# Kernel optimization log

Hardware: AMD Instinct MI355X
Metric: run time of the kernel (lower is better)

The kernel has to match this reference:

```python
import jax, jax.numpy as jnp
import numpy as np

D_MODEL = 1024
N_HEADS = 16
D_K = D_MODEL // N_HEADS
LN_EPS = 1e-5


def setup_inputs() -> dict:
    key = jax.random.key(0)
    ks = jax.random.split(key, 8)
    B, Sq, Skv = 2, 2048, 2048
    scale = 1.0 / np.sqrt(D_MODEL)
    return {
        "query": jax.random.normal(ks[0], (B, Sq, D_MODEL), dtype=jnp.float32),
        "key_value": jax.random.normal(ks[1], (B, Skv, D_MODEL), dtype=jnp.float32),
        "W_qkv": jax.random.normal(ks[2], (3 * D_MODEL, D_MODEL), dtype=jnp.float32) * scale,
        "b_qkv": jax.random.normal(ks[3], (3 * D_MODEL,), dtype=jnp.float32) * 0.01,
        "W_o": jax.random.normal(ks[4], (D_MODEL, D_MODEL), dtype=jnp.float32) * scale,
        "b_o": jax.random.normal(ks[5], (D_MODEL,), dtype=jnp.float32) * 0.01,
        "ln_gamma": jnp.ones((D_MODEL,), dtype=jnp.float32),
        "ln_beta": jnp.zeros((D_MODEL,), dtype=jnp.float32),
    }


def _attention(query, key_value, W_qkv, b_qkv, W_o, b_o, ln_gamma, ln_beta):
    B, Sq, _ = query.shape
    Skv = key_value.shape[1]
    # Q from query rows of qkv_proj; K,V from key_value rows (slice weights -> same
    # math as projecting then slicing, without the discarded 2/3 and 1/3 compute).
    Wq, Wk, Wv = W_qkv[:D_MODEL], W_qkv[D_MODEL:2 * D_MODEL], W_qkv[2 * D_MODEL:]
    bq, bk, bv = b_qkv[:D_MODEL], b_qkv[D_MODEL:2 * D_MODEL], b_qkv[2 * D_MODEL:]
    Q = (query @ Wq.T + bq).reshape(B, Sq, N_HEADS, D_K).transpose(0, 2, 1, 3)
    K = (key_value @ Wk.T + bk).reshape(B, Skv, N_HEADS, D_K).transpose(0, 2, 1, 3)
    V = (key_value @ Wv.T + bv).reshape(B, Skv, N_HEADS, D_K).transpose(0, 2, 1, 3)
    # fp32 attention (original forces float32 inside autocast(enabled=False))
    scores = jnp.einsum('bhqd,bhkd->bhqk', Q.astype(jnp.float32), K.astype(jnp.float32))
    scores = scores / np.sqrt(D_K)
    attn = jax.nn.softmax(scores, axis=-1)  # dropout is identity at inference
    context = jnp.einsum('bhqk,bhkd->bhqd', attn, V.astype(jnp.float32)).astype(query.dtype)
    context = context.transpose(0, 2, 1, 3).reshape(B, Sq, D_MODEL)
    output = context @ W_o.T + b_o
    # residual + LayerNorm
    x = output + query
    mu = jnp.mean(x, axis=-1, keepdims=True)
    var = jnp.mean(jnp.square(x - mu), axis=-1, keepdims=True)
    return (x - mu) / jnp.sqrt(var + LN_EPS) * ln_gamma + ln_beta


def reference(query, key_value, W_qkv, b_qkv, W_o, b_o, ln_gamma, ln_beta):
    return _attention(query, key_value, W_qkv, b_qkv, W_o, b_o, ln_gamma, ln_beta)
```

## Files before the change

### kernel.cpp

```cpp
#include <hip/hip_runtime.h>
#include <hip/hip_bf16.h>

typedef __attribute__((ext_vector_type(4))) float f32x4;
typedef __attribute__((ext_vector_type(16))) float f32x16;
typedef __attribute__((ext_vector_type(8))) __bf16 bf16x8;
typedef __attribute__((ext_vector_type(2))) __bf16 bf16x2;

#define DEV __device__ __forceinline__

DEV unsigned short f2bf(float f) {
    union { float f; unsigned u; } x; x.f = f;
    unsigned r = x.u + 0x7fffu + ((x.u >> 16) & 1u);
    return (unsigned short)(r >> 16);
}

DEV unsigned packbf(float a, float b) {
    union { bf16x2 h; unsigned u; } t;
    t.h[0] = (__bf16)a; t.h[1] = (__bf16)b;
    return t.u;
}

DEV float bflo(unsigned u) { union { unsigned u; float f; } x; x.u = u << 16; return x.f; }
DEV float bfhi(unsigned u) { union { unsigned u; float f; } x; x.u = u & 0xffff0000u; return x.f; }

DEV void gload16(const void* g, void* l) {
    __builtin_amdgcn_global_load_lds(
        (const __attribute__((address_space(1))) void*)g,
        (__attribute__((address_space(3))) void*)l, 16, 0, 0);
}

#define PLSWAP(a, b) asm("v_permlane32_swap_b32 %0, %1" : "+v"(a), "+v"(b))

DEV bf16x8 ldsfrag(const unsigned short* base, int row, int kcol) {
    int byte = (row << 7) + (kcol << 1);
    byte ^= (row & 7) << 4;
    return *reinterpret_cast<const bf16x8*>(reinterpret_cast<const char*>(base) + byte);
}

__global__ __launch_bounds__(256) void cvt_all(
    const float* __restrict__ q, const float* __restrict__ kv,
    const float* __restrict__ wq, const float* __restrict__ wo,
    unsigned short* __restrict__ qb, unsigned short* __restrict__ kvb,
    unsigned short* __restrict__ wqb, unsigned short* __restrict__ wob)
{
    int i = blockIdx.x * 256 + threadIdx.x;
    const float* s; unsigned short* d; int o;
    if (i < 2097152) {
        if (i < 1048576) { s = q;  d = qb;  o = i; }
        else             { s = kv; d = kvb; o = i - 1048576; }
    } else {
        if (i < 2883584) { s = wq; d = wqb; o = i - 2097152; }
        else             { s = wo; d = wob; o = i - 2883584; }
    }
    f32x4 v = *reinterpret_cast<const f32x4*>(s + (size_t)o * 4);
    ushort4 u;
    u.x = f2bf(v.x); u.y = f2bf(v.y); u.z = f2bf(v.z); u.w = f2bf(v.w);
    *reinterpret_cast<ushort4*>(d + (size_t)o * 4) = u;
}

__global__ __launch_bounds__(256) void gemm_qkv(
    const unsigned short* __restrict__ Aq,
    const unsigned short* __restrict__ Akv,
    const unsigned short* __restrict__ W,
    const float* __restrict__ bias,
    unsigned short* __restrict__ QP,
    unsigned short* __restrict__ KP,
    unsigned short* __restrict__ VP)
{
    __shared__ unsigned short lA[2][128 * 64];
    __shared__ unsigned short lB[2][128 * 64];
    int xcd = blockIdx.x & 7, idx = blockIdx.x >> 3;
    int bm = ((xcd >> 1) << 3) + (idx & 7);
    int bn = (xcd & 1) * 12 + (idx >> 3);
    int m0 = bm * 128, n0 = bn * 128;
    const unsigned short* A = (bn < 8) ? Aq : Akv;
    int tid = threadIdx.x, lane = tid & 63, wv = tid >> 6;
    int wm = (wv >> 1) * 64, wn = (wv & 1) * 64;
    int cg = lane >> 4, cl = lane & 15;

    const unsigned short* sA[4];
    const unsigned short* sB[4];
#pragma unroll
    for (int p = 0; p < 4; ++p) {
        int o = p * 4096 + tid * 16;
        int r = o >> 7;
        int c = ((o ^ ((r & 7) << 4)) >> 1) & 63;
        sA[p] = A + (size_t)(m0 + r) * 1024 + c;
        sB[p] = W + (size_t)(n0 + r) * 1024 + c;
    }
    const int dl = wv * 1024;

    auto STAGE = [&](int buf, int k0) {
#pragma unroll
        for (int p = 0; p < 4; ++p) {
            gload16(sA[p] + k0, (char*)lA[buf] + p * 4096 + dl);
            gload16(sB[p] + k0, (char*)lB[buf] + p * 4096 + dl);
        }
    };

    f32x4 acc[4][4] = {};

    STAGE(0, 0);
    for (int kt = 0; kt < 16; ++kt) {
        const int cur = kt & 1;
        if (kt < 15) {
            STAGE(cur ^ 1, (kt + 1) * 64);
            asm volatile("s_waitcnt vmcnt(8)" ::: "memory");
        } else {
            asm volatile("s_waitcnt vmcnt(0)" ::: "memory");
        }
        __builtin_amdgcn_s_barrier();
#pragma unroll
        for (int ks = 0; ks < 2; ++ks) {
            bf16x8 af[4], bfr[4];
#pragma unroll
            for (int i = 0; i < 4; ++i) af[i] = ldsfrag(lA[cur], wm + i * 16 + cl, ks * 32 + cg * 8);
#pragma unroll
            for (int j = 0; j < 4; ++j) bfr[j] = ldsfrag(lB[cur], wn + j * 16 + cl, ks * 32 + cg * 8);
#pragma unroll
            for (int i = 0; i < 4; ++i)
#pragma unroll
                for (int j = 0; j < 4; ++j)
                    acc[i][j] = __builtin_amdgcn_mfma_f32_16x16x32_bf16(af[i], bfr[j], acc[i][j], 0, 0, 0);
        }
        asm volatile("s_waitcnt lgkmcnt(0)" ::: "memory");
        __builtin_amdgcn_s_barrier();
    }

    unsigned short* img = (unsigned short*)lA;
    const int which = (bn >= 16) ? 2 : (bn >= 8 ? 1 : 0);
    const float scale = (which == 0) ? 0.18033688f : 1.0f;

#pragma unroll
    for (int j = 0; j < 4; ++j) {
        int nn = wn + j * 16 + cl;
        int d = nn & 63, chunk = nn >> 6;
        float bv = bias[n0 + nn];
#pragma unroll
        for (int i = 0; i < 4; ++i) {
#pragma unroll
            for (int r = 0; r < 4; ++r) {
                int mm = wm + i * 16 + cg * 4 + r;
                float v = (acc[i][j][r] + bv) * scale;
                int off;
                if (which < 2)
                    off = ((mm >> 5) * 4 + (d >> 4)) * 512
                        + (((d >> 3) & 1) * 32 + (mm & 31)) * 8 + (d & 7);
                else
                    off = (((mm >> 6) * 2 + (d >> 5)) * 4 + ((mm >> 4) & 3)) * 512
                        + (((mm >> 3) & 1) * 32 + (d & 31)) * 8 + (mm & 7);
                img[chunk * 8192 + off] = f2bf(v);
            }
        }
    }
    __syncthreads();

    int bb = m0 >> 11, s0 = m0 & 2047;
    int h0 = (bn & 7) * 2;
    unsigned short* dst[2];
#pragma unroll
    for (int c = 0; c < 2; ++c) {
        int bh = bb * 16 + h0 + c;
        if (which == 0)      dst[c] = QP + ((size_t)bh * 64 + (s0 >> 5)) * 2048;
        else if (which == 1) dst[c] = KP + ((size_t)bh * 64 + (s0 >> 5)) * 2048;
        else                 dst[c] = VP + ((size_t)bh * 32 + (s0 >> 6)) * 4096;
    }
#pragma unroll
    for (int c = 0; c < 2; ++c)
#pragma unroll
        for (int k = 0; k < 4; ++k) {
            int e = (k * 256 + tid) * 8;
            *reinterpret_cast<uint4*>(dst[c] + e) =
                *reinterpret_cast<const uint4*>(img + c * 8192 + e);
        }
}

__global__ __launch_bounds__(256, 2) void attn(
    const unsigned short* __restrict__ QP,
    const unsigned short* __restrict__ KP,
    const unsigned short* __restrict__ VP,
    unsigned short* __restrict__ OP,
    float2* __restrict__ ML)
{
    int swz = (blockIdx.x & 7) * 64 + (blockIdx.x >> 3);
    int bh = swz >> 4;
    int qc = (swz >> 1) & 7;
    int spl = swz & 1;
    int tid = threadIdx.x, lane = tid & 63, wv = tid >> 6;
    int ql = lane & 31, hh = lane >> 5;
    int qs = qc * 256 + wv * 64;
    const unsigned short* kp = KP + (size_t)bh * 131072 + lane * 8;
    const unsigned short* vp = VP + (size_t)bh * 131072 + lane * 8;
    const int tbase = spl * 16;

    bf16x8 qfA[4], qfB[4];
    {
        const unsigned short* qpA = QP + ((size_t)(bh * 64 + (qs >> 5)) * 4) * 512 + lane * 8;
#pragma unroll
        for (int ks = 0; ks < 4; ++ks) {
            qfA[ks] = *reinterpret_cast<const bf16x8*>(qpA + ks * 512);
            qfB[ks] = *reinterpret_cast<const bf16x8*>(qpA + 2048 + ks * 512);
        }
    }

    bf16x8 ka[4], kc[4], va[4], vc[4];
    auto LOADK = [&](int t) {
        const unsigned short* b = kp + (size_t)t * 4096;
#pragma unroll
        for (int ks = 0; ks < 4; ++ks) {
            ka[ks] = *reinterpret_cast<const bf16x8*>(b + ks * 512);
            kc[ks] = *reinterpret_cast<const bf16x8*>(b + 2048 + ks * 512);
        }
    };
    auto LOADV = [&](int t) {
        const unsigned short* b = vp + (size_t)t * 4096;
#pragma unroll
        for (int kh = 0; kh < 4; ++kh) {
            va[kh] = *reinterpret_cast<const bf16x8*>(b + kh * 512);
            vc[kh] = *reinterpret_cast<const bf16x8*>(b + 2048 + kh * 512);
        }
    };

    f32x16 oA0 = {}, oA1 = {}, oB0 = {}, oB1 = {};
    f32x4 psA = {0.f, 0.f, 0.f, 0.f}, psB = {0.f, 0.f, 0.f, 0.f};

    auto EXPPACK = [&](f32x16& s0, f32x16& s1, unsigned (&pb)[4][4], f32x4& psa) {
#pragma unroll
        for (int r = 0; r < 16; r += 4) {
            s0[r]     = __builtin_amdgcn_exp2f(s0[r]);     psa[0] += s0[r];
            s0[r + 1] = __builtin_amdgcn_exp2f(s0[r + 1]); psa[1] += s0[r + 1];
            s0[r + 2] = __builtin_amdgcn_exp2f(s0[r + 2]); psa[2] += s0[r + 2];
            s0[r + 3] = __builtin_amdgcn_exp2f(s0[r + 3]); psa[3] += s0[r + 3];
        }
#pragma unroll
        for (int r = 0; r < 16; r += 4) {
            s1[r]     = __builtin_amdgcn_exp2f(s1[r]);     psa[0] += s1[r];
            s1[r + 1] = __builtin_amdgcn_exp2f(s1[r + 1]); psa[1] += s1[r + 1];
            s1[r + 2] = __builtin_amdgcn_exp2f(s1[r + 2]); psa[2] += s1[r + 2];
            s1[r + 3] = __builtin_amdgcn_exp2f(s1[r + 3]); psa[3] += s1[r + 3];
        }
        unsigned A0 = packbf(s0[0], s0[1]),   B0 = packbf(s0[2], s0[3]);
        unsigned C0 = packbf(s0[4], s0[5]),   D0 = packbf(s0[6], s0[7]);
        unsigned E0 = packbf(s0[8], s0[9]),   F0 = packbf(s0[10], s0[11]);
        unsigned G0 = packbf(s0[12], s0[13]), H0 = packbf(s0[14], s0[15]);
        unsigned A1 = packbf(s1[0], s1[1]),   B1 = packbf(s1[2], s1[3]);
        unsigned C1 = packbf(s1[4], s1[5]),   D1 = packbf(s1[6], s1[7]);
        unsigned E1 = packbf(s1[8], s1[9]),   F1 = packbf(s1[10], s1[11]);
        unsigned G1 = packbf(s1[12], s1[13]), H1 = packbf(s1[14], s1[15]);
        PLSWAP(A0, C0); PLSWAP(B0, D0); PLSWAP(E0, G0); PLSWAP(F0, H0);
        PLSWAP(A1, C1); PLSWAP(B1, D1); PLSWAP(E1, G1); PLSWAP(F1, H1);
        pb[0][0] = A0; pb[0][1] = B0; pb[0][2] = C0; pb[0][3] = D0;
        pb[1][0] = E0; pb[1][1] = F0; pb[1][2] = G0; pb[1][3] = H0;
        pb[2][0] = A1; pb[2][1] = B1; pb[2][2] = C1; pb[2][3] = D1;
        pb[3][0] = E1; pb[3][1] = F1; pb[3][2] = G1; pb[3][3] = H1;
    };

    LOADK(tbase);
    LOADV(tbase);
    for (int t = 0; t < 16; ++t) {
        f32x16 sA0 = {}, sA1 = {};
        __builtin_amdgcn_s_setprio(1);
#pragma unroll
        for (int ks = 0; ks < 4; ++ks) {
            sA0 = __builtin_amdgcn_mfma_f32_32x32x16_bf16(ka[ks], qfA[ks], sA0, 0, 0, 0);
            sA1 = __builtin_amdgcn_mfma_f32_32x32x16_bf16(kc[ks], qfA[ks], sA1, 0, 0, 0);
        }
        __builtin_amdgcn_s_setprio(0);
        unsigned pbA[4][4];
        EXPPACK(sA0, sA1, pbA, psA);
        f32x16 sB0 = {}, sB1 = {};
        __builtin_amdgcn_s_setprio(1);
#pragma unroll
        for (int ks = 0; ks < 4; ++ks) {
            sB0 = __builtin_amdgcn_mfma_f32_32x32x16_bf16(ka[ks], qfB[ks], sB0, 0, 0, 0);
            sB1 = __builtin_amdgcn_mfma_f32_32x32x16_bf16(kc[ks], qfB[ks], sB1, 0, 0, 0);
        }
        __builtin_amdgcn_s_setprio(0);
        LOADK(tbase + t + 1);
        __builtin_amdgcn_s_setprio(1);
#pragma unroll
        for (int kh = 0; kh < 4; ++kh) {
            union { unsigned u[4]; bf16x8 v; } pa;
            pa.u[0] = pbA[kh][0]; pa.u[1] = pbA[kh][1];
            pa.u[2] = pbA[kh][2]; pa.u[3] = pbA[kh][3];
            oA0 = __builtin_amdgcn_mfma_f32_32x32x16_bf16(va[kh], pa.v, oA0, 0, 0, 0);
            oA1 = __builtin_amdgcn_mfma_f32_32x32x16_bf16(vc[kh], pa.v, oA1, 0, 0, 0);
        }
        __builtin_amdgcn_s_setprio(0);
        unsigned pbB[4][4];
        EXPPACK(sB0, sB1, pbB, psB);
        __builtin_amdgcn_s_setprio(1);
#pragma unroll
        for (int kh = 0; kh < 4; ++kh) {
            union { unsigned u[4]; bf16x8 v; } pc;
            pc.u[0] = pbB[kh][0]; pc.u[1] = pbB[kh][1];
            pc.u[2] = pbB[kh][2]; pc.u[3] = pbB[kh][3];
            oB0 = __builtin_amdgcn_mfma_f32_32x32x16_bf16(va[kh], pc.v, oB0, 0, 0, 0);
            oB1 = __builtin_amdgcn_mfma_f32_32x32x16_bf16(vc[kh], pc.v, oB1, 0, 0, 0);
        }
        __builtin_amdgcn_s_setprio(0);
        LOADV(tbase + t + 1);
    }

    float lA = (psA[0] + psA[1]) + (psA[2] + psA[3]);
    float lB = (psB[0] + psB[1]) + (psB[2] + psB[3]);
    float lAx = lA, lBx = lB;
    PLSWAP(lA, lAx); PLSWAP(lB, lBx);
    lA += lAx; lB += lBx;

    size_t rowA = (size_t)(spl * 32 + bh) * 2048 + qs + ql;
    size_t rowB = rowA + 32;
    if (hh == 0) {
        ML[rowA] = make_float2(0.0f, lA);
        ML[rowB] = make_float2(0.0f, lB);
    }
    float invA = 1.0f / lA, invB = 1.0f / lB;
    unsigned short* cpA = OP + rowA * 64 + hh * 4;
    unsigned short* cpB = OP + rowB * 64 + hh * 4;
#pragma unroll
    for (int m = 0; m < 4; ++m) {
        uint2 w0, w1;
        w0.x = packbf(oA0[4 * m] * invA, oA0[4 * m + 1] * invA);
        w0.y = packbf(oA0[4 * m + 2] * invA, oA0[4 * m + 3] * invA);
        w1.x = packbf(oA1[4 * m] * invA, oA1[4 * m + 1] * invA);
        w1.y = packbf(oA1[4 * m + 2] * invA, oA1[4 * m + 3] * invA);
        *reinterpret_cast<uint2*>(cpA + 8 * m) = w0;
        *reinterpret_cast<uint2*>(cpA + 32 + 8 * m) = w1;
        w0.x = packbf(oB0[4 * m] * invB, oB0[4 * m + 1] * invB);
        w0.y = packbf(oB0[4 * m + 2] * invB, oB0[4 * m + 3] * invB);
        w1.x = packbf(oB1[4 * m] * invB, oB1[4 * m + 1] * invB);
        w1.y = packbf(oB1[4 * m + 2] * invB, oB1[4 * m + 3] * invB);
        *reinterpret_cast<uint2*>(cpB + 8 * m) = w0;
        *reinterpret_cast<uint2*>(cpB + 32 + 8 * m) = w1;
    }
}

__global__ __launch_bounds__(256) void combine(
    const unsigned short* __restrict__ OP,
    const float2* __restrict__ ML,
    unsigned short* __restrict__ ctx)
{
    int row = blockIdx.x * 256 + threadIdx.x;
    int bh = row >> 11, q = row & 2047;
    float2 ml1 = ML[row];
    float2 ml2 = ML[65536 + row];
    float M = fmaxf(ml1.x, ml2.x);
    float w1 = ml1.y * __builtin_amdgcn_exp2f(ml1.x - M);
    float w2 = ml2.y * __builtin_amdgcn_exp2f(ml2.x - M);
    float inv = 1.0f / (w1 + w2);
    w1 *= inv; w2 *= inv;
    const unsigned short* p1 = OP + (size_t)row * 64;
    const unsigned short* p2 = OP + ((size_t)65536 + row) * 64;
    int b = bh >> 4, h = bh & 15;
    unsigned short* op = ctx + (size_t)(b * 2048 + q) * 1024 + h * 64;
#pragma unroll
    for (int c = 0; c < 8; ++c) {
        uint4 u1 = *reinterpret_cast<const uint4*>(p1 + c * 8);
        uint4 u2 = *reinterpret_cast<const uint4*>(p2 + c * 8);
        uint4 r;
        r.x = packbf(bflo(u1.x) * w1 + bflo(u2.x) * w2, bfhi(u1.x) * w1 + bfhi(u2.x) * w2);
        r.y = packbf(bflo(u1.y) * w1 + bflo(u2.y) * w2, bfhi(u1.y) * w1 + bfhi(u2.y) * w2);
        r.z = packbf(bflo(u1.z) * w1 + bflo(u2.z) * w2, bfhi(u1.z) * w1 + bfhi(u2.z) * w2);
        r.w = packbf(bflo(u1.w) * w1 + bflo(u2.w) * w2, bfhi(u1.w) * w1 + bfhi(u2.w) * w2);
        *reinterpret_cast<uint4*>(op + c * 8) = r;
    }
}

__global__ __launch_bounds__(256) void gemm_out(
    const unsigned short* __restrict__ A,
    const unsigned short* __restrict__ W,
    const float* __restrict__ bo,
    const float* __restrict__ resid,
    float* __restrict__ X)
{
    __shared__ unsigned short lA[3][64 * 64];
    __shared__ unsigned short lB[3][128 * 64];
    int bn = blockIdx.x & 7, bm = blockIdx.x >> 3;
    int m0 = bm * 64, n0 = bn * 128;
    int tid = threadIdx.x, lane = tid & 63, wv = tid >> 6;
    int wm = (wv >> 1) * 32, wn = (wv & 1) * 64;
    int cg = lane >> 4, cl = lane & 15;

    const unsigned short* sA[2];
    const unsigned short* sB[4];
#pragma unroll
    for (int p = 0; p < 2; ++p) {
        int o = p * 4096 + tid * 16;
        int r = o >> 7;
        int c = ((o ^ ((r & 7) << 4)) >> 1) & 63;
        sA[p] = A + (size_t)(m0 + r) * 1024 + c;
    }
#pragma unroll
    for (int p = 0; p < 4; ++p) {
        int o = p * 4096 + tid * 16;
        int r = o >> 7;
        int c = ((o ^ ((r & 7) << 4)) >> 1) & 63;
        sB[p] = W + (size_t)(n0 + r) * 1024 + c;
    }
    const int dl = wv * 1024;

    auto STAGE = [&](int buf, int k0) {
#pragma unroll
        for (int p = 0; p < 2; ++p)
            gload16(sA[p] + k0, (char*)lA[buf] + p * 4096 + dl);
#pragma unroll
        for (int p = 0; p < 4; ++p)
            gload16(sB[p] + k0, (char*)lB[buf] + p * 4096 + dl);
    };

    f32x4 acc[2][4] = {};

    STAGE(0, 0);
    STAGE(1, 64);
    int cur = 0;
    for (int kt = 0; kt < 16; ++kt) {
        __builtin_amdgcn_s_barrier();
        if (kt < 14) {
            int nb = (cur >= 1) ? cur - 1 : 2;
            STAGE(nb, (kt + 2) * 64);
            asm volatile("s_waitcnt vmcnt(12)" ::: "memory");
        } else if (kt == 14) {
            asm volatile("s_waitcnt vmcnt(6)" ::: "memory");
        } else {
            asm volatile("s_waitcnt vmcnt(0)" ::: "memory");
        }
#pragma unroll
        for (int ks = 0; ks < 2; ++ks) {
            bf16x8 af[2], bfr[4];
#pragma unroll
            for (int i = 0; i < 2; ++i) af[i] = ldsfrag(lA[cur], wm + i * 16 + cl, ks * 32 + cg * 8);
#pragma unroll
            for (int j = 0; j < 4; ++j) bfr[j] = ldsfrag(lB[cur], wn + j * 16 + cl, ks * 32 + cg * 8);
#pragma unroll
            for (int i = 0; i < 2; ++i)
#pragma unroll
                for (int j = 0; j < 4; ++j)
                    acc[i][j] = __builtin_amdgcn_mfma_f32_16x16x32_bf16(af[i], bfr[j], acc[i][j], 0, 0, 0);
        }
        cur = (cur == 2) ? 0 : cur + 1;
    }

#pragma unroll
    for (int j = 0; j < 4; ++j) {
        int n = n0 + wn + j * 16 + cl;
        float bv = bo[n];
#pragma unroll
        for (int i = 0; i < 2; ++i)
#pragma unroll
            for (int r = 0; r < 4; ++r) {
                int m = m0 + wm + i * 16 + cg * 4 + r;
                size_t idx = (size_t)m * 1024 + n;
                X[idx] = acc[i][j][r] + bv + resid[idx];
            }
    }
}

__global__ __launch_bounds__(256) void ln_k(float* __restrict__ X,
                                            const float* __restrict__ gam,
                                            const float* __restrict__ bet)
{
    __shared__ float red[8];
    int row = blockIdx.x, tid = threadIdx.x;
    int lane = tid & 63, wv = tid >> 6;
    f32x4 v = *reinterpret_cast<const f32x4*>(X + (size_t)row * 1024 + tid * 4);
    float s = (v.x + v.y) + (v.z + v.w);
#pragma unroll
    for (int m = 32; m >= 1; m >>= 1) s += __shfl_xor(s, m, 64);
    if (lane == 0) red[wv] = s;
    __syncthreads();
    float mu = (red[0] + red[1] + red[2] + red[3]) * (1.0f / 1024.0f);
    f32x4 d = v - mu;
    float sq = (d.x * d.x + d.y * d.y) + (d.z * d.z + d.w * d.w);
#pragma unroll
    for (int m = 32; m >= 1; m >>= 1) sq += __shfl_xor(sq, m, 64);
    if (lane == 0) red[4 + wv] = sq;
    __syncthreads();
    float var = (red[4] + red[5] + red[6] + red[7]) * (1.0f / 1024.0f);
    float rstd = rsqrtf(var + 1e-5f);
    f32x4 gg = *reinterpret_cast<const f32x4*>(gam + tid * 4);
    f32x4 bb = *reinterpret_cast<const f32x4*>(bet + tid * 4);
    f32x4 y;
    y.x = d.x * rstd * gg.x + bb.x;
    y.y = d.y * rstd * gg.y + bb.y;
    y.z = d.z * rstd * gg.z + bb.z;
    y.w = d.w * rstd * gg.w + bb.w;
    *reinterpret_cast<f32x4*>(X + (size_t)row * 1024 + tid * 4) = y;
}

extern "C" void kernel_launch(void* const* d_in, const int* in_sizes, int n_in,
                              void* d_out, int out_size, void* d_ws, size_t ws_size,
                              hipStream_t stream) {
    const float* query     = (const float*)d_in[0];
    const float* key_value = (const float*)d_in[1];
    const float* W_qkv     = (const float*)d_in[2];
    const float* b_qkv     = (const float*)d_in[3];
    const float* W_o       = (const float*)d_in[4];
    const float* b_o       = (const float*)d_in[5];
    const float* ln_gamma  = (const float*)d_in[6];
    const float* ln_beta   = (const float*)d_in[7];
    float* out = (float*)d_out;

    char* ws = (char*)d_ws;
    const size_t MB = 1u << 20;
    unsigned short* qb   = (unsigned short*)(ws + 0 * MB);
    unsigned short* kvb  = (unsigned short*)(ws + 8 * MB);
    unsigned short* wqb  = (unsigned short*)(ws + 16 * MB);
    unsigned short* wob  = (unsigned short*)(ws + 22 * MB);
    unsigned short* QP   = (unsigned short*)(ws + 24 * MB);
    unsigned short* KP   = (unsigned short*)(ws + 32 * MB);
    unsigned short* VP   = (unsigned short*)(ws + 40 * MB);
    unsigned short* ctx  = (unsigned short*)(ws + 48 * MB);
    unsigned short* OP   = (unsigned short*)(ws + 0 * MB);
    float2*         ML   = (float2*)(ws + 20 * MB);

    (void)in_sizes; (void)n_in; (void)out_size; (void)ws_size;

    cvt_all<<<12288, 256, 0, stream>>>(query, key_value, W_qkv, W_o, qb, kvb, wqb, wob);

    gemm_qkv<<<32 * 24, 256, 0, stream>>>(qb, kvb, wqb, b_qkv, QP, KP, VP);
    attn<<<512, 256, 0, stream>>>(QP, KP, VP, OP, ML);
    combine<<<256, 256, 0, stream>>>(OP, ML, ctx);
    gemm_out<<<512, 256, 0, stream>>>(ctx, wob, b_o, query, out);
    ln_k<<<4096, 256, 0, stream>>>(out, ln_gamma, ln_beta);
}
```

Baseline: 133.7 us.

## Enlarge QKV GEMM tiles to 256x256 with 512 threads and interleaved prefetch

The QKV projection GEMM moves from 128x128 tiles with 256 threads to 256x256 tiles with 512 threads, launched as 192 blocks. Global-to-LDS staging of the next K slice is now split into pieces and interleaved with the MFMA sub-steps, with barriers and s_setprio raising priority around the MFMA groups. The goal is more data reuse per tile and better overlap of loads with math. The cost is 128KB of LDS per block and a grid smaller than the CU count, which may leave some CUs idle. The epilogue's LDS re-layout and stores are generalised to four heads per tile.

```diff
diff --git a/kernel.cpp b/kernel.cpp
--- a/kernel.cpp
+++ b/kernel.cpp
@@ -58,7 +58,7 @@
     *reinterpret_cast<ushort4*>(d + (size_t)o * 4) = u;
 }
 
-__global__ __launch_bounds__(256) void gemm_qkv(
+__global__ __launch_bounds__(512, 2) void gemm_qkv(
     const unsigned short* __restrict__ Aq,
     const unsigned short* __restrict__ Akv,
     const unsigned short* __restrict__ W,
@@ -67,77 +67,94 @@
     unsigned short* __restrict__ KP,
     unsigned short* __restrict__ VP)
 {
-    __shared__ unsigned short lA[2][128 * 64];
-    __shared__ unsigned short lB[2][128 * 64];
+    __shared__ unsigned short lds[65536];
     int xcd = blockIdx.x & 7, idx = blockIdx.x >> 3;
-    int bm = ((xcd >> 1) << 3) + (idx & 7);
-    int bn = (xcd & 1) * 12 + (idx >> 3);
-    int m0 = bm * 128, n0 = bn * 128;
-    const unsigned short* A = (bn < 8) ? Aq : Akv;
+    int hi = (idx >= 12) ? 1 : 0;
+    int bm = (xcd << 1) + hi;
+    int bn = idx - hi * 12;
+    int m0 = bm * 256, n0 = bn * 256;
+    const unsigned short* A = (bn < 4) ? Aq : Akv;
     int tid = threadIdx.x, lane = tid & 63, wv = tid >> 6;
-    int wm = (wv >> 1) * 64, wn = (wv & 1) * 64;
+    int wm = (wv >> 2) * 128, wn = (wv & 3) * 64;
     int cg = lane >> 4, cl = lane & 15;
 
     const unsigned short* sA[4];
     const unsigned short* sB[4];
 #pragma unroll
     for (int p = 0; p < 4; ++p) {
-        int o = p * 4096 + tid * 16;
+        int o = p * 8192 + tid * 16;
         int r = o >> 7;
         int c = ((o ^ ((r & 7) << 4)) >> 1) & 63;
         sA[p] = A + (size_t)(m0 + r) * 1024 + c;
         sB[p] = W + (size_t)(n0 + r) * 1024 + c;
     }
+    char* lbase = (char*)lds;
     const int dl = wv * 1024;
 
-    auto STAGE = [&](int buf, int k0) {
-#pragma unroll
-        for (int p = 0; p < 4; ++p) {
-            gload16(sA[p] + k0, (char*)lA[buf] + p * 4096 + dl);
-            gload16(sB[p] + k0, (char*)lB[buf] + p * 4096 + dl);
-        }
+    auto STAGE1 = [&](int buf, int p, int kt) {
+        const int k0 = kt * 64;
+        gload16(sA[p] + k0, lbase + buf * 32768 + p * 8192 + dl);
+        gload16(sB[p] + k0, lbase + 65536 + buf * 32768 + p * 8192 + dl);
     };
 
-    f32x4 acc[4][4] = {};
-
-    STAGE(0, 0);
-    for (int kt = 0; kt < 16; ++kt) {
-        const int cur = kt & 1;
-        if (kt < 15) {
-            STAGE(cur ^ 1, (kt + 1) * 64);
-            asm volatile("s_waitcnt vmcnt(8)" ::: "memory");
-        } else {
-            asm volatile("s_waitcnt vmcnt(0)" ::: "memory");
-        }
-        __builtin_amdgcn_s_barrier();
-#pragma unroll
-        for (int ks = 0; ks < 2; ++ks) {
-            bf16x8 af[4], bfr[4];
-#pragma unroll
-            for (int i = 0; i < 4; ++i) af[i] = ldsfrag(lA[cur], wm + i * 16 + cl, ks * 32 + cg * 8);
-#pragma unroll
-            for (int j = 0; j < 4; ++j) bfr[j] = ldsfrag(lB[cur], wn + j * 16 + cl, ks * 32 + cg * 8);
+    f32x4 acc[8][4] = {};
+
+#pragma unroll
+    for (int p = 0; p < 4; ++p) STAGE1(0, p, 0);
+    asm volatile("s_waitcnt vmcnt(0)" ::: "memory");
+    __builtin_amdgcn_s_barrier();
+
+    for (int c = 0; c < 16; ++c) {
+        const int buf = c & 1;
+        const unsigned short* la = lds + buf * 16384;
+        const unsigned short* lb = lds + 32768 + buf * 16384;
+        bf16x8 bfr[4];
+#pragma unroll
+        for (int q = 0; q < 4; ++q) {
+            if (c < 15 && q < 2) {
+                STAGE1(buf ^ 1, 2 * q, c + 1);
+                STAGE1(buf ^ 1, 2 * q + 1, c + 1);
+            }
+            const int ks = q >> 1, ih = (q & 1) * 4;
+            if ((q & 1) == 0) {
+#pragma unroll
+                for (int j = 0; j < 4; ++j)
+                    bfr[j] = ldsfrag(lb, wn + j * 16 + cl, ks * 32 + cg * 8);
+            }
+            bf16x8 af[4];
 #pragma unroll
             for (int i = 0; i < 4; ++i)
+                af[i] = ldsfrag(la, wm + (ih + i) * 16 + cl, ks * 32 + cg * 8);
+            __builtin_amdgcn_s_barrier();
+            __builtin_amdgcn_s_setprio(1);
+#pragma unroll
+            for (int i = 0; i < 4; ++i)
 #pragma unroll
                 for (int j = 0; j < 4; ++j)
-                    acc[i][j] = __builtin_amdgcn_mfma_f32_16x16x32_bf16(af[i], bfr[j], acc[i][j], 0, 0, 0);
-        }
-        asm volatile("s_waitcnt lgkmcnt(0)" ::: "memory");
-        __builtin_amdgcn_s_barrier();
-    }
-
-    unsigned short* img = (unsigned short*)lA;
-    const int which = (bn >= 16) ? 2 : (bn >= 8 ? 1 : 0);
+                    acc[ih + i][j] = __builtin_amdgcn_mfma_f32_16x16x32_bf16(
+                        af[i], bfr[j], acc[ih + i][j], 0, 0, 0);
+            __builtin_amdgcn_s_setprio(0);
+            if (q == 3) {
+                asm volatile("s_waitcnt lgkmcnt(0)" ::: "memory");
+                asm volatile("s_waitcnt vmcnt(0)" ::: "memory");
+            }
+            __builtin_amdgcn_s_barrier();
+        }
+    }
+    __syncthreads();
+
+    unsigned short* img = (unsigned short*)lds;
+    const int which = bn >> 2;
     const float scale = (which == 0) ? 0.18033688f : 1.0f;
+    const int chunk = wv & 3;
+    unsigned short* imgc = img + chunk * 16384;
 
 #pragma unroll
     for (int j = 0; j < 4; ++j) {
-        int nn = wn + j * 16 + cl;
-        int d = nn & 63, chunk = nn >> 6;
-        float bv = bias[n0 + nn];
-#pragma unroll
-        for (int i = 0; i < 4; ++i) {
+        int d = j * 16 + cl;
+        float bv = bias[n0 + wn + d];
+#pragma unroll
+        for (int i = 0; i < 8; ++i) {
 #pragma unroll
             for (int r = 0; r < 4; ++r) {
                 int mm = wm + i * 16 + cg * 4 + r;
@@ -149,30 +166,28 @@
                 else
                     off = (((mm >> 6) * 2 + (d >> 5)) * 4 + ((mm >> 4) & 3)) * 512
                         + (((mm >> 3) & 1) * 32 + (d & 31)) * 8 + (mm & 7);
-                img[chunk * 8192 + off] = f2bf(v);
+                imgc[off] = f2bf(v);
             }
         }
     }
     __syncthreads();
 
     int bb = m0 >> 11, s0 = m0 & 2047;
-    int h0 = (bn & 7) * 2;
-    unsigned short* dst[2];
-#pragma unroll
-    for (int c = 0; c < 2; ++c) {
-        int bh = bb * 16 + h0 + c;
-        if (which == 0)      dst[c] = QP + ((size_t)bh * 64 + (s0 >> 5)) * 2048;
-        else if (which == 1) dst[c] = KP + ((size_t)bh * 64 + (s0 >> 5)) * 2048;
-        else                 dst[c] = VP + ((size_t)bh * 32 + (s0 >> 6)) * 4096;
-    }
-#pragma unroll
-    for (int c = 0; c < 2; ++c)
+    int h0 = (bn & 3) * 4;
+#pragma unroll
+    for (int cc = 0; cc < 4; ++cc) {
+        int bh = bb * 16 + h0 + cc;
+        unsigned short* dst;
+        if (which == 0)      dst = QP + ((size_t)bh * 64 + (s0 >> 5)) * 2048;
+        else if (which == 1) dst = KP + ((size_t)bh * 64 + (s0 >> 5)) * 2048;
+        else                 dst = VP + ((size_t)bh * 32 + (s0 >> 6)) * 4096;
 #pragma unroll
         for (int k = 0; k < 4; ++k) {
-            int e = (k * 256 + tid) * 8;
-            *reinterpret_cast<uint4*>(dst[c] + e) =
-                *reinterpret_cast<const uint4*>(img + c * 8192 + e);
-        }
+            int e = (k * 512 + tid) * 8;
+            *reinterpret_cast<uint4*>(dst + e) =
+                *reinterpret_cast<const uint4*>(img + cc * 16384 + e);
+        }
+    }
 }
 
 __global__ __launch_bounds__(256, 2) void attn(
@@ -517,7 +532,7 @@
 
     cvt_all<<<12288, 256, 0, stream>>>(query, key_value, W_qkv, W_o, qb, kvb, wqb, wob);
 
-    gemm_qkv<<<32 * 24, 256, 0, stream>>>(qb, kvb, wqb, b_qkv, QP, KP, VP);
+    gemm_qkv<<<192, 512, 0, stream>>>(qb, kvb, wqb, b_qkv, QP, KP, VP);
     attn<<<512, 256, 0, stream>>>(QP, KP, VP, OP, ML);
     combine<<<256, 256, 0, stream>>>(OP, ML, ctx);
     gemm_out<<<512, 256, 0, stream>>>(ctx, wob, b_o, query, out);
```

Result: faster. 125.3 us (-6.3%).
